# Optimization experiments

Hardware: AMD Instinct MI355X
Metric: run time of the kernel (lower is better)

## Reference

```python
import jax, jax.numpy as jnp
import numpy as np

B, S, D_MODEL, H = 2, 2048, 1024, 16
HD = D_MODEL // H  # 64
THETA = 10000.0


def setup_inputs() -> dict:
    key = jax.random.key(0)
    ks = jax.random.split(key, 5)
    std = (2.0 / (D_MODEL + D_MODEL)) ** 0.5
    x = jax.random.normal(ks[0], (B, S, D_MODEL), dtype=jnp.float32)
    Wq = jax.random.normal(ks[1], (D_MODEL, D_MODEL), dtype=jnp.float32) * std
    Wk = jax.random.normal(ks[2], (D_MODEL, D_MODEL), dtype=jnp.float32) * std
    Wv = jax.random.normal(ks[3], (D_MODEL, D_MODEL), dtype=jnp.float32) * std
    Wo = jax.random.normal(ks[4], (D_MODEL, D_MODEL), dtype=jnp.float32) * std
    # RoPE tables (buffers)
    pos = jnp.arange(S, dtype=jnp.float32)
    freq = THETA ** (-jnp.arange(0, HD, 2, dtype=jnp.float32) / HD)  # [HD/2]
    ang = jnp.outer(pos, freq)  # [S, HD/2]
    token_positions = jnp.arange(S, dtype=jnp.int32)
    return {
        "x": x,
        "token_positions": token_positions,
        "use_rope": 1,
        "Wq": Wq, "Wk": Wk, "Wv": Wv, "Wo": Wo,
        "cos": jnp.cos(ang), "sin": jnp.sin(ang),
    }


def _apply_rope(t, c, sn):
    # t: [b,h,s,d]; c,sn: [s,d/2] (broadcast over b,h)
    e = t[..., 0::2]
    o = t[..., 1::2]
    return jnp.stack([e * c - o * sn, o * c + e * sn], axis=-1).reshape(t.shape)


def reference(x, token_positions, use_rope, Wq, Wk, Wv, Wo, cos, sin):
    b, s, _ = x.shape

    def split_heads(t):  # [b,s,D] -> [b,h,s,hd]
        return t.reshape(b, s, H, HD).transpose(0, 2, 1, 3)

    q = split_heads(x @ Wq.T)
    k = split_heads(x @ Wk.T)
    v = split_heads(x @ Wv.T)

    if use_rope:
        c = cos[token_positions]   # [s, hd/2]
        sn = sin[token_positions]  # [s, hd/2]
        q = _apply_rope(q, c, sn)
        k = _apply_rope(k, c, sn)

    scale = 1.0 / jnp.sqrt(jnp.float32(HD))
    scores = jnp.einsum('bhqd,bhkd->bhqk', q, k) * scale  # [b,h,s,s]
    causal = jnp.tril(jnp.ones((s, s), dtype=bool))
    scores = jnp.where(causal, scores, -jnp.inf)
    attn = jax.nn.softmax(scores, axis=-1)
    y = jnp.einsum('bhqk,bhkd->bhqd', attn, v)
    y = y.transpose(0, 2, 1, 3).reshape(b, s, D_MODEL)
    return y @ Wo.T
```

## Files before the change

kernel.cpp:

```cpp
#include <hip/hip_runtime.h>
#include <math.h>

#define BB 2
#define SS 2048
#define DM 1024
#define NH 16
#define HD 64

typedef __attribute__((ext_vector_type(8))) __bf16 bf16x8;
typedef __attribute__((ext_vector_type(4))) __bf16 bf16x4;
typedef __attribute__((ext_vector_type(8))) unsigned short u16x8;
typedef __attribute__((ext_vector_type(4))) float f32x4;
typedef unsigned short u16;
typedef unsigned int u32;
typedef __attribute__((address_space(1))) unsigned int u32g;
typedef __attribute__((address_space(3))) unsigned int u32l;

#define CEXP 0.18033688011112042f

static __device__ __forceinline__ u16 f2bf(float f) {
    __bf16 h = (__bf16)f;
    return __builtin_bit_cast(unsigned short, h);
}

static __device__ __forceinline__ void gld16(const u16* g, u16* l) {
    __builtin_amdgcn_global_load_lds((const u32g*)g, (u32l*)l, 16, 0, 0);
}

__global__ __launch_bounds__(256)
void cast_all(const float* __restrict__ x,
              const float* __restrict__ wq, const float* __restrict__ wk,
              const float* __restrict__ wv, const float* __restrict__ wo,
              u16* __restrict__ xb, u16* __restrict__ wqb, u16* __restrict__ wkb,
              u16* __restrict__ wvb, u16* __restrict__ wob)
{
    const int N4X = (BB * SS * DM) / 4;
    const int N4W = (DM * DM) / 4;
    int i = blockIdx.x * 256 + threadIdx.x;
    const float* src; u16* dst; int off;
    if (i < N4X) { src = x; dst = xb; off = i; }
    else {
        int i2 = i - N4X;
        int w = i2 >> 18;
        off = i2 & (N4W - 1);
        switch (w) {
            case 0:  src = wq; dst = wqb; break;
            case 1:  src = wk; dst = wkb; break;
            case 2:  src = wv; dst = wvb; break;
            default: src = wo; dst = wob; break;
        }
    }
    float4 v = ((const float4*)src)[off];
    ushort4 o;
    o.x = f2bf(v.x); o.y = f2bf(v.y); o.z = f2bf(v.z); o.w = f2bf(v.w);
    ((ushort4*)dst)[off] = o;
}

__global__ __launch_bounds__(256, 3)
void qkv_gemm(const u16* __restrict__ X,
              const u16* __restrict__ Wq, const u16* __restrict__ Wk,
              const u16* __restrict__ Wv,
              const int* __restrict__ tp, const float* __restrict__ cosp,
              const float* __restrict__ sinp, const int* __restrict__ use_rope,
              u16* __restrict__ Q, u16* __restrict__ K, u16* __restrict__ V)
{
    const u16* W; u16* dst;
    if (blockIdx.z == 0)      { W = Wq; dst = Q; }
    else if (blockIdx.z == 1) { W = Wk; dst = K; }
    else                      { W = Wv; dst = V; }

    __shared__ u16 SH[4 * 64 * 68];
    u16* As = SH;
    u16* Bs = SH + 8192;
    const int t  = threadIdx.x;
    const int wv = t >> 6, L = t & 63, ln = L & 15, qd = L >> 4;
    const int i0 = blockIdx.y * 128, j0 = blockIdx.x * 128;
    const int wm = (wv >> 1) * 64, wn = (wv & 1) * 64;
    const int srow = L >> 3;
    const int scg  = ((L & 7) ^ (L >> 3)) * 8;

    f32x4 acc[4][4];
    #pragma unroll
    for (int a = 0; a < 4; ++a)
        #pragma unroll
        for (int b = 0; b < 4; ++b)
            #pragma unroll
            for (int e = 0; e < 4; ++e) acc[a][b][e] = 0.f;

    for (int k0 = 0; k0 < DM; k0 += 64) {
        __syncthreads();
        #pragma unroll
        for (int g = 0; g < 4; ++g) {
            int rb = wv * 32 + g * 8;
            gld16(X + (size_t)(i0 + rb + srow) * DM + k0 + scg, &As[rb * 64]);
            gld16(W + (size_t)(j0 + rb + srow) * DM + k0 + scg, &Bs[rb * 64]);
        }
        __syncthreads();
        bf16x8 a[4][2], b[4][2];
        #pragma unroll
        for (int mi = 0; mi < 4; ++mi)
            #pragma unroll
            for (int kd = 0; kd < 2; ++kd)
                a[mi][kd] = *(const bf16x8*)&As[(wm + mi * 16 + ln) * 64 + (((kd * 4 + qd) ^ (ln & 7)) * 8)];
        #pragma unroll
        for (int ni = 0; ni < 4; ++ni)
            #pragma unroll
            for (int kd = 0; kd < 2; ++kd)
                b[ni][kd] = *(const bf16x8*)&Bs[(wn + ni * 16 + ln) * 64 + (((kd * 4 + qd) ^ (ln & 7)) * 8)];
        #pragma unroll
        for (int kd = 0; kd < 2; ++kd)
            #pragma unroll
            for (int mi = 0; mi < 4; ++mi)
                #pragma unroll
                for (int ni = 0; ni < 4; ++ni)
                    acc[mi][ni] = __builtin_amdgcn_mfma_f32_16x16x32_bf16(a[mi][kd], b[ni][kd], acc[mi][ni], 0, 0, 0);
    }

    const int rope_on = (blockIdx.z < 2) ? use_rope[0] : 0;
    if (rope_on) {
        #pragma unroll
        for (int mi = 0; mi < 4; ++mi)
            #pragma unroll
            for (int r = 0; r < 4; ++r) {
                int gi = i0 + wm + mi * 16 + qd * 4 + r;
                int s = gi & 2047;
                int pos = tp[s];
                #pragma unroll
                for (int ni = 0; ni < 4; ++ni) {
                    int d = wn + ni * 16 + ln;
                    int dh = d & 63;
                    float c  = cosp[pos * 32 + (dh >> 1)];
                    float sn = sinp[pos * 32 + (dh >> 1)];
                    float v = acc[mi][ni][r];
                    float pv = __shfl_xor(v, 1);
                    acc[mi][ni][r] = (dh & 1) ? (v * c + pv * sn) : (v * c - pv * sn);
                }
            }
    }

    __syncthreads();
    u16* Ts = SH + wv * (64 * 68);
    #pragma unroll
    for (int mi = 0; mi < 4; ++mi)
        #pragma unroll
        for (int ni = 0; ni < 4; ++ni)
            #pragma unroll
            for (int r = 0; r < 4; ++r)
                Ts[(mi * 16 + qd * 4 + r) * 68 + ni * 16 + ln] = f2bf(acc[mi][ni][r]);

    const int h  = blockIdx.x * 2 + (wv & 1);
    const int sb = i0 + wm;
    const int b_ = sb >> 11, s0 = sb & 2047;
    if (blockIdx.z < 2) {
        const int lrow = L >> 3, lcol = (L & 7) * 8;
        #pragma unroll
        for (int r2 = 0; r2 < 8; ++r2) {
            int row = lrow + r2 * 8;
            u16x8 val = *(const u16x8*)&Ts[row * 68 + lcol];
            *(u16x8*)&dst[(((size_t)(b_ * NH + h)) * SS + s0 + row) * HD + lcol] = val;
        }
    } else {
        const int sch = (L & 7) * 8;
        const int dr0 = L >> 3;
        #pragma unroll
        for (int r2 = 0; r2 < 8; ++r2) {
            int d = dr0 + r2 * 8;
            u16x8 val;
            #pragma unroll
            for (int u = 0; u < 8; ++u) val[u] = Ts[(sch + u) * 68 + d];
            *(u16x8*)&dst[(((size_t)(b_ * NH + h)) * HD + d) * SS + s0 + sch] = val;
        }
    }
}

__global__ __launch_bounds__(512, 2)
void out_gemm(const u16* __restrict__ X, const u16* __restrict__ W,
              float* __restrict__ dst)
{
    __shared__ char SHB[73728];
    u16* As = (u16*)SHB;
    u16* Bs = (u16*)SHB + 8192;
    const int t  = threadIdx.x;
    const int wv = t >> 6, L = t & 63, ln = L & 15, qd = L >> 4;
    const int i0 = blockIdx.y * 128, j0 = blockIdx.x * 128;
    const int wm = (wv >> 2) * 64, wn = (wv & 3) * 32;
    const int srow = L >> 3;
    const int scg  = ((L & 7) ^ (L >> 3)) * 8;

    f32x4 acc[4][2];
    #pragma unroll
    for (int mi = 0; mi < 4; ++mi)
        #pragma unroll
        for (int ni = 0; ni < 2; ++ni)
            #pragma unroll
            for (int e = 0; e < 4; ++e) acc[mi][ni][e] = 0.f;

    for (int k0 = 0; k0 < DM; k0 += 64) {
        __syncthreads();
        #pragma unroll
        for (int g = 0; g < 2; ++g) {
            int rb = wv * 16 + g * 8;
            gld16(X + (size_t)(i0 + rb + srow) * DM + k0 + scg, &As[rb * 64]);
            gld16(W + (size_t)(j0 + rb + srow) * DM + k0 + scg, &Bs[rb * 64]);
        }
        __syncthreads();
        bf16x8 a[4][2], b[2][2];
        #pragma unroll
        for (int mi = 0; mi < 4; ++mi)
            #pragma unroll
            for (int kd = 0; kd < 2; ++kd)
                a[mi][kd] = *(const bf16x8*)&As[(wm + mi * 16 + ln) * 64 + (((kd * 4 + qd) ^ (ln & 7)) * 8)];
        #pragma unroll
        for (int ni = 0; ni < 2; ++ni)
            #pragma unroll
            for (int kd = 0; kd < 2; ++kd)
                b[ni][kd] = *(const bf16x8*)&Bs[(wn + ni * 16 + ln) * 64 + (((kd * 4 + qd) ^ (ln & 7)) * 8)];
        #pragma unroll
        for (int kd = 0; kd < 2; ++kd)
            #pragma unroll
            for (int mi = 0; mi < 4; ++mi)
                #pragma unroll
                for (int ni = 0; ni < 2; ++ni)
                    acc[mi][ni] = __builtin_amdgcn_mfma_f32_16x16x32_bf16(a[mi][kd], b[ni][kd], acc[mi][ni], 0, 0, 0);
    }

    __syncthreads();
    float* Ts = (float*)SHB + wv * (64 * 36);
    #pragma unroll
    for (int mi = 0; mi < 4; ++mi)
        #pragma unroll
        for (int ni = 0; ni < 2; ++ni)
            #pragma unroll
            for (int r = 0; r < 4; ++r)
                Ts[(mi * 16 + qd * 4 + r) * 36 + ni * 16 + ln] = acc[mi][ni][r];

    const int lrow = L >> 3, lch = L & 7;
    #pragma unroll
    for (int r2 = 0; r2 < 8; ++r2) {
        int row = lrow + r2 * 8;
        float4 v = *(const float4*)&Ts[row * 36 + lch * 4];
        *(float4*)&dst[(size_t)(i0 + wm + row) * DM + j0 + wn + lch * 4] = v;
    }
}

static __device__ __forceinline__ void group_step(
    const u16* KsB, const bf16x8 qf[2], u16* psw,
    bool diag, int rowg, int j0, int ln, int qd,
    float& m, float& l, bf16x8& pf0, bf16x8& pf1)
{
    const int pm = 2 * (ln & 7);
    f32x4 s[4];
    __builtin_amdgcn_s_setprio(1);
    #pragma unroll
    for (int mt = 0; mt < 4; ++mt) {
        bf16x8 a0 = *(const bf16x8*)&KsB[(mt * 16 + ln) * 64 + ((qd ^ (ln & 7)) * 8)];
        bf16x8 a1 = *(const bf16x8*)&KsB[(mt * 16 + ln) * 64 + (((4 + qd) ^ (ln & 7)) * 8)];
        #pragma unroll
        for (int e = 0; e < 4; ++e) s[mt][e] = 0.f;
        s[mt] = __builtin_amdgcn_mfma_f32_16x16x32_bf16(a0, qf[0], s[mt], 0, 0, 0);
        s[mt] = __builtin_amdgcn_mfma_f32_16x16x32_bf16(a1, qf[1], s[mt], 0, 0, 0);
    }
    __builtin_amdgcn_s_setprio(0);
    if (diag) {
        #pragma unroll
        for (int mt = 0; mt < 4; ++mt)
            #pragma unroll
            for (int r = 0; r < 4; ++r)
                if (j0 + mt * 16 + qd * 4 + r > rowg) s[mt][r] = -3.0e38f;
    }

    float p[16];
    float nmc = m * CEXP;
    #pragma unroll
    for (int mt = 0; mt < 4; ++mt)
        #pragma unroll
        for (int r = 0; r < 4; ++r)
            p[mt * 4 + r] = exp2f(fmaf(s[mt][r], CEXP, -nmc));

    float rm = s[0][0];
    #pragma unroll
    for (int mt = 0; mt < 4; ++mt)
        #pragma unroll
        for (int r = 0; r < 4; ++r) rm = fmaxf(rm, s[mt][r]);
    rm = fmaxf(rm, __shfl_xor(rm, 16));
    rm = fmaxf(rm, __shfl_xor(rm, 32));

    if (__any((rm - m) * CEXP > 8.0f)) {
        float nm = fmaxf(m, rm);
        float alpha = exp2f((m - nm) * CEXP);
        nmc = nm * CEXP;
        #pragma unroll
        for (int mt = 0; mt < 4; ++mt)
            #pragma unroll
            for (int r = 0; r < 4; ++r)
                p[mt * 4 + r] = exp2f(fmaf(s[mt][r], CEXP, -nmc));
        l *= alpha;
        m = nm;
    }

    float rs = 0.f;
    #pragma unroll
    for (int mt = 0; mt < 4; ++mt) {
        bf16x4 pk;
        #pragma unroll
        for (int r = 0; r < 4; ++r) {
            rs += p[mt * 4 + r];
            pk[r] = (__bf16)p[mt * 4 + r];
        }
        *(bf16x4*)(psw + ln * 64 + ((mt * 4 + qd) ^ pm) * 4) = pk;
    }
    rs += __shfl_xor(rs, 16);
    rs += __shfl_xor(rs, 32);
    l += rs;
    pf0 = *(const bf16x8*)(psw + ln * 64 + ((qd * 2) ^ pm) * 4);
    pf1 = *(const bf16x8*)(psw + ln * 64 + ((8 + qd * 2) ^ pm) * 4);
}

__global__ __launch_bounds__(512, 4)
void attn_kernel(const u16* __restrict__ Q, const u16* __restrict__ K,
                 const u16* __restrict__ V, u16* __restrict__ Y)
{
    __shared__ u16 Ks[2][64 * 64];
    __shared__ u16 Vt[2][64 * 64];
    __shared__ u16 Ps[8][16 * 64];

    const int t  = threadIdx.x;
    const int wv = t >> 6, L = t & 63, ln = L & 15, qd = L >> 4;
    const int wsub = wv & 3, grp = wv >> 2;
    const int bh = blockIdx.x;
    const int y = blockIdx.y;
    const int p = (y < 8) ? y : (23 - y);
    const int qb = (grp ? (31 - p) : p) * 64;
    const u16* Qp = Q + (size_t)bh * SS * HD;
    const u16* Kp = K + (size_t)bh * SS * HD;
    const u16* Vp = V + (size_t)bh * HD * SS;
    const int srow = L >> 3;
    const int scg  = ((L & 7) ^ (L >> 3)) * 8;

    const int ntile   = 32 - p;
    const int myTiles = grp ? ntile : (p + 1);

    bf16x8 qf[2];
    {
        const u16* rq = Qp + (size_t)(qb + wsub * 16 + ln) * HD;
        qf[0] = *(const bf16x8*)(rq + qd * 8);
        qf[1] = *(const bf16x8*)(rq + 32 + qd * 8);
    }

    f32x4 o[4];
    #pragma unroll
    for (int ni = 0; ni < 4; ++ni)
        #pragma unroll
        for (int e = 0; e < 4; ++e) o[ni][e] = 0.f;
    float m = -3.0e38f, l = 0.f;

    gld16(Kp + (size_t)(wv * 8 + srow) * HD + scg, &Ks[0][(wv * 8) * 64]);
    gld16(Vp + (size_t)(wv * 8 + srow) * SS + scg, &Vt[0][(wv * 8) * 64]);
    __syncthreads();

    for (int tix = 0; tix < ntile; ++tix) {
        const int j0 = tix * 64;
        const int buf = tix & 1;
        const bool more = (tix + 1 < ntile);

        if (more) {
            const int j1 = j0 + 64;
            gld16(Kp + (size_t)(j1 + wv * 8 + srow) * HD + scg, &Ks[buf ^ 1][(wv * 8) * 64]);
            gld16(Vp + (size_t)(wv * 8 + srow) * SS + j1 + scg, &Vt[buf ^ 1][(wv * 8) * 64]);
        }

        if (tix < myTiles) {
            bf16x8 vf[2][4];
            #pragma unroll
            for (int kc = 0; kc < 2; ++kc)
                #pragma unroll
                for (int ni = 0; ni < 4; ++ni)
                    vf[kc][ni] = *(const bf16x8*)&Vt[buf][(ni * 16 + ln) * 64 + (((kc * 4 + qd) ^ (ln & 7)) * 8)];

            float m_old = m;
            bf16x8 pf0, pf1;
            group_step(Ks[buf], qf, &Ps[wv][0], tix == myTiles - 1,
                       qb + wsub * 16 + ln, j0, ln, qd, m, l, pf0, pf1);
            if (m != m_old) {
                float alpha = exp2f((m_old - m) * CEXP);
                #pragma unroll
                for (int ni = 0; ni < 4; ++ni)
                    #pragma unroll
                    for (int r = 0; r < 4; ++r) o[ni][r] *= alpha;
            }
            __builtin_amdgcn_s_setprio(1);
            #pragma unroll
            for (int ni = 0; ni < 4; ++ni)
                o[ni] = __builtin_amdgcn_mfma_f32_16x16x32_bf16(vf[0][ni], pf0, o[ni], 0, 0, 0);
            #pragma unroll
            for (int ni = 0; ni < 4; ++ni)
                o[ni] = __builtin_amdgcn_mfma_f32_16x16x32_bf16(vf[1][ni], pf1, o[ni], 0, 0, 0);
            __builtin_amdgcn_s_setprio(0);
        }
        __syncthreads();
    }

    const int b = bh >> 4, h = bh & 15;
    const float inv = 1.f / l;
    const int sq = qb + wsub * 16 + ln;
    #pragma unroll
    for (int ni = 0; ni < 4; ++ni) {
        bf16x4 pk;
        #pragma unroll
        for (int r = 0; r < 4; ++r) pk[r] = (__bf16)(o[ni][r] * inv);
        *(bf16x4*)&Y[((size_t)(b * SS + sq)) * DM + h * HD + ni * 16 + qd * 4] = pk;
    }
}

extern "C" void kernel_launch(void* const* d_in, const int* in_sizes, int n_in,
                              void* d_out, int out_size, void* d_ws, size_t ws_size,
                              hipStream_t stream)
{
    const float* x        = (const float*)d_in[0];
    const int*   tp       = (const int*)d_in[1];
    const int*   use_rope = (const int*)d_in[2];
    const float* Wq       = (const float*)d_in[3];
    const float* Wk       = (const float*)d_in[4];
    const float* Wv       = (const float*)d_in[5];
    const float* Wo       = (const float*)d_in[6];
    const float* cosp     = (const float*)d_in[7];
    const float* sinp     = (const float*)d_in[8];
    float* out = (float*)d_out;

    char* ws = (char*)d_ws;
    const size_t MB = 1 << 20;
    u16* xb  = (u16*)(ws);
    u16* Wqb = (u16*)(ws + 8 * MB);
    u16* Wkb = (u16*)(ws + 10 * MB);
    u16* Wvb = (u16*)(ws + 12 * MB);
    u16* Wob = (u16*)(ws + 14 * MB);
    u16* Qb  = (u16*)(ws + 16 * MB);
    u16* Kb  = (u16*)(ws + 24 * MB);
    u16* Vb  = (u16*)(ws + 32 * MB);
    u16* Yb  = (u16*)(ws + 40 * MB);

    cast_all<<<8192, 256, 0, stream>>>(x, Wq, Wk, Wv, Wo, xb, Wqb, Wkb, Wvb, Wob);
    qkv_gemm<<<dim3(DM / 128, BB * SS / 128, 3), 256, 0, stream>>>(
        xb, Wqb, Wkb, Wvb, tp, cosp, sinp, use_rope, Qb, Kb, Vb);
    attn_kernel<<<dim3(BB * NH, 16), 512, 0, stream>>>(Qb, Kb, Vb, Yb);
    out_gemm<<<dim3(DM / 128, BB * SS / 128), 512, 0, stream>>>(Yb, Wob, out);
}
```

Baseline: 183.2 us.

## Split causal attention KV range across paired waves and read K/V directly

Each wave now owns a 16-row query strip. It processes the first half of the KV tiles for one strip and the second half for the mirrored strip. Partial softmax state (m, l, O) goes to shared memory and is merged with a partner wave, which balances causal work per wave. The double-buffered LDS staging of K and V tiles is removed in favour of direct global/L1 loads, and the grid becomes 32×32 blocks of 256 threads. This trades away the shared-memory reuse and prefetch overlap, exposing more global-load latency, in exchange for finer-grained, better-balanced work and lower LDS usage.

```diff
diff --git a/kernel.cpp b/kernel.cpp
--- a/kernel.cpp
+++ b/kernel.cpp
@@ -243,24 +243,23 @@
     }
 }
 
-static __device__ __forceinline__ void group_step(
-    const u16* KsB, const bf16x8 qf[2], u16* psw,
-    bool diag, int rowg, int j0, int ln, int qd,
-    float& m, float& l, bf16x8& pf0, bf16x8& pf1)
+static __device__ __forceinline__ void attn_tile(
+    const u16* __restrict__ Kp, const u16* __restrict__ Vp,
+    bf16x8 qf0, bf16x8 qf1, u16* psw,
+    int j0, bool diag, int rowg, int ln, int qd,
+    float& m, float& l, f32x4* o)
 {
     const int pm = 2 * (ln & 7);
     f32x4 s[4];
-    __builtin_amdgcn_s_setprio(1);
+    const u16* kb = Kp + (size_t)(j0 + ln) * HD + qd * 8;
     #pragma unroll
     for (int mt = 0; mt < 4; ++mt) {
-        bf16x8 a0 = *(const bf16x8*)&KsB[(mt * 16 + ln) * 64 + ((qd ^ (ln & 7)) * 8)];
-        bf16x8 a1 = *(const bf16x8*)&KsB[(mt * 16 + ln) * 64 + (((4 + qd) ^ (ln & 7)) * 8)];
-        #pragma unroll
-        for (int e = 0; e < 4; ++e) s[mt][e] = 0.f;
-        s[mt] = __builtin_amdgcn_mfma_f32_16x16x32_bf16(a0, qf[0], s[mt], 0, 0, 0);
-        s[mt] = __builtin_amdgcn_mfma_f32_16x16x32_bf16(a1, qf[1], s[mt], 0, 0, 0);
-    }
-    __builtin_amdgcn_s_setprio(0);
+        bf16x8 a0 = *(const bf16x8*)(kb + mt * 16 * HD);
+        bf16x8 a1 = *(const bf16x8*)(kb + mt * 16 * HD + 32);
+        s[mt][0] = s[mt][1] = s[mt][2] = s[mt][3] = 0.f;
+        s[mt] = __builtin_amdgcn_mfma_f32_16x16x32_bf16(a0, qf0, s[mt], 0, 0, 0);
+        s[mt] = __builtin_amdgcn_mfma_f32_16x16x32_bf16(a1, qf1, s[mt], 0, 0, 0);
+    }
     if (diag) {
         #pragma unroll
         for (int mt = 0; mt < 4; ++mt)
@@ -294,6 +293,10 @@
             #pragma unroll
             for (int r = 0; r < 4; ++r)
                 p[mt * 4 + r] = exp2f(fmaf(s[mt][r], CEXP, -nmc));
+        #pragma unroll
+        for (int ni = 0; ni < 4; ++ni)
+            #pragma unroll
+            for (int r = 0; r < 4; ++r) o[ni][r] *= alpha;
         l *= alpha;
         m = nm;
     }
@@ -312,103 +315,94 @@
     rs += __shfl_xor(rs, 16);
     rs += __shfl_xor(rs, 32);
     l += rs;
-    pf0 = *(const bf16x8*)(psw + ln * 64 + ((qd * 2) ^ pm) * 4);
-    pf1 = *(const bf16x8*)(psw + ln * 64 + ((8 + qd * 2) ^ pm) * 4);
-}
-
-__global__ __launch_bounds__(512, 4)
+    bf16x8 pf0 = *(const bf16x8*)(psw + ln * 64 + ((qd * 2) ^ pm) * 4);
+    bf16x8 pf1 = *(const bf16x8*)(psw + ln * 64 + ((8 + qd * 2) ^ pm) * 4);
+
+    const u16* vb = Vp + (size_t)ln * SS + j0 + qd * 8;
+    #pragma unroll
+    for (int ni = 0; ni < 4; ++ni) {
+        bf16x8 vf0 = *(const bf16x8*)(vb + (size_t)(ni * 16) * SS);
+        bf16x8 vf1 = *(const bf16x8*)(vb + (size_t)(ni * 16) * SS + 32);
+        o[ni] = __builtin_amdgcn_mfma_f32_16x16x32_bf16(vf0, pf0, o[ni], 0, 0, 0);
+        o[ni] = __builtin_amdgcn_mfma_f32_16x16x32_bf16(vf1, pf1, o[ni], 0, 0, 0);
+    }
+}
+
+__global__ __launch_bounds__(256, 4)
 void attn_kernel(const u16* __restrict__ Q, const u16* __restrict__ K,
                  const u16* __restrict__ V, u16* __restrict__ Y)
 {
-    __shared__ u16 Ks[2][64 * 64];
-    __shared__ u16 Vt[2][64 * 64];
-    __shared__ u16 Ps[8][16 * 64];
+    __shared__ u16  Ps[4][16 * 64];
+    __shared__ float MO[4][16 * 64];
+    __shared__ float ML[4][32];
 
     const int t  = threadIdx.x;
     const int wv = t >> 6, L = t & 63, ln = L & 15, qd = L >> 4;
-    const int wsub = wv & 3, grp = wv >> 2;
-    const int bh = blockIdx.x;
-    const int y = blockIdx.y;
-    const int p = (y < 8) ? y : (23 - y);
-    const int qb = (grp ? (31 - p) : p) * 64;
+    const int bh = blockIdx.x, b2 = blockIdx.y;
+    const int b  = bh >> 4, h = bh & 15;
     const u16* Qp = Q + (size_t)bh * SS * HD;
     const u16* Kp = K + (size_t)bh * SS * HD;
     const u16* Vp = V + (size_t)bh * HD * SS;
-    const int srow = L >> 3;
-    const int scg  = ((L & 7) ^ (L >> 3)) * 8;
-
-    const int ntile   = 32 - p;
-    const int myTiles = grp ? ntile : (p + 1);
-
-    bf16x8 qf[2];
+
+    const int s1 = (wv == 0) ? 2 * b2 : (wv == 1) ? 2 * b2 + 1
+                 : (wv == 2) ? 126 - 2 * b2 : 127 - 2 * b2;
+    const int s2 = 127 - s1;
+    const int T1 = (s1 >> 2) + 1, T2 = (s2 >> 2) + 1;
+
+    u16* psw = &Ps[wv][0];
+    float m, l;
+    f32x4 o[4];
+
     {
-        const u16* rq = Qp + (size_t)(qb + wsub * 16 + ln) * HD;
-        qf[0] = *(const bf16x8*)(rq + qd * 8);
-        qf[1] = *(const bf16x8*)(rq + 32 + qd * 8);
-    }
-
-    f32x4 o[4];
-    #pragma unroll
-    for (int ni = 0; ni < 4; ++ni)
-        #pragma unroll
-        for (int e = 0; e < 4; ++e) o[ni][e] = 0.f;
-    float m = -3.0e38f, l = 0.f;
-
-    gld16(Kp + (size_t)(wv * 8 + srow) * HD + scg, &Ks[0][(wv * 8) * 64]);
-    gld16(Vp + (size_t)(wv * 8 + srow) * SS + scg, &Vt[0][(wv * 8) * 64]);
+        const int qb = s1 * 16;
+        const u16* rq = Qp + (size_t)(qb + ln) * HD;
+        bf16x8 qf0 = *(const bf16x8*)(rq + qd * 8);
+        bf16x8 qf1 = *(const bf16x8*)(rq + 32 + qd * 8);
+        m = -3.0e38f; l = 0.f;
+        #pragma unroll
+        for (int ni = 0; ni < 4; ++ni)
+            o[ni][0] = o[ni][1] = o[ni][2] = o[ni][3] = 0.f;
+        const int e1 = T1 >> 1;
+        #pragma unroll 1
+        for (int tix = 0; tix < e1; ++tix)
+            attn_tile(Kp, Vp, qf0, qf1, psw, tix * 64, false, qb + ln, ln, qd, m, l, o);
+        if (qd == 0) { ML[wv][ln] = m; ML[wv][16 + ln] = l; }
+        #pragma unroll
+        for (int ni = 0; ni < 4; ++ni)
+            *(f32x4*)&MO[wv][ln * 64 + (((ni * 4 + qd) ^ ln) * 4)] = o[ni];
+    }
+
+    {
+        const int qb = s2 * 16;
+        const u16* rq = Qp + (size_t)(qb + ln) * HD;
+        bf16x8 qf0 = *(const bf16x8*)(rq + qd * 8);
+        bf16x8 qf1 = *(const bf16x8*)(rq + 32 + qd * 8);
+        m = -3.0e38f; l = 0.f;
+        #pragma unroll 1
+        for (int tix = T2 >> 1; tix < T2; ++tix)
+            attn_tile(Kp, Vp, qf0, qf1, psw, tix * 64, tix == T2 - 1, qb + ln, ln, qd, m, l, o);
+    }
+
     __syncthreads();
 
-    for (int tix = 0; tix < ntile; ++tix) {
-        const int j0 = tix * 64;
-        const int buf = tix & 1;
-        const bool more = (tix + 1 < ntile);
-
-        if (more) {
-            const int j1 = j0 + 64;
-            gld16(Kp + (size_t)(j1 + wv * 8 + srow) * HD + scg, &Ks[buf ^ 1][(wv * 8) * 64]);
-            gld16(Vp + (size_t)(wv * 8 + srow) * SS + j1 + scg, &Vt[buf ^ 1][(wv * 8) * 64]);
-        }
-
-        if (tix < myTiles) {
-            bf16x8 vf[2][4];
-            #pragma unroll
-            for (int kc = 0; kc < 2; ++kc)
-                #pragma unroll
-                for (int ni = 0; ni < 4; ++ni)
-                    vf[kc][ni] = *(const bf16x8*)&Vt[buf][(ni * 16 + ln) * 64 + (((kc * 4 + qd) ^ (ln & 7)) * 8)];
-
-            float m_old = m;
-            bf16x8 pf0, pf1;
-            group_step(Ks[buf], qf, &Ps[wv][0], tix == myTiles - 1,
-                       qb + wsub * 16 + ln, j0, ln, qd, m, l, pf0, pf1);
-            if (m != m_old) {
-                float alpha = exp2f((m_old - m) * CEXP);
-                #pragma unroll
-                for (int ni = 0; ni < 4; ++ni)
-                    #pragma unroll
-                    for (int r = 0; r < 4; ++r) o[ni][r] *= alpha;
-            }
-            __builtin_amdgcn_s_setprio(1);
-            #pragma unroll
-            for (int ni = 0; ni < 4; ++ni)
-                o[ni] = __builtin_amdgcn_mfma_f32_16x16x32_bf16(vf[0][ni], pf0, o[ni], 0, 0, 0);
-            #pragma unroll
-            for (int ni = 0; ni < 4; ++ni)
-                o[ni] = __builtin_amdgcn_mfma_f32_16x16x32_bf16(vf[1][ni], pf1, o[ni], 0, 0, 0);
-            __builtin_amdgcn_s_setprio(0);
-        }
-        __syncthreads();
-    }
-
-    const int b = bh >> 4, h = bh & 15;
-    const float inv = 1.f / l;
-    const int sq = qb + wsub * 16 + ln;
-    #pragma unroll
-    for (int ni = 0; ni < 4; ++ni) {
-        bf16x4 pk;
-        #pragma unroll
-        for (int r = 0; r < 4; ++r) pk[r] = (__bf16)(o[ni][r] * inv);
-        *(bf16x4*)&Y[((size_t)(b * SS + sq)) * DM + h * HD + ni * 16 + qd * 4] = pk;
+    {
+        const int pw = 3 - wv;
+        float mp = ML[pw][ln], lp = ML[pw][16 + ln];
+        float mf = fmaxf(m, mp);
+        float as = exp2f((m - mf) * CEXP);
+        float ap = exp2f((mp - mf) * CEXP);
+        float lf = as * l + ap * lp;
+        float inv = 1.f / lf;
+        const int sq = s2 * 16 + ln;
+        #pragma unroll
+        for (int ni = 0; ni < 4; ++ni) {
+            f32x4 op = *(const f32x4*)&MO[pw][ln * 64 + (((ni * 4 + qd) ^ ln) * 4)];
+            bf16x4 pk;
+            #pragma unroll
+            for (int r = 0; r < 4; ++r)
+                pk[r] = (__bf16)((as * o[ni][r] + ap * op[r]) * inv);
+            *(bf16x4*)&Y[((size_t)(b * SS + sq)) * DM + h * HD + ni * 16 + qd * 4] = pk;
+        }
     }
 }
 
@@ -442,6 +436,6 @@
     cast_all<<<8192, 256, 0, stream>>>(x, Wq, Wk, Wv, Wo, xb, Wqb, Wkb, Wvb, Wob);
     qkv_gemm<<<dim3(DM / 128, BB * SS / 128, 3), 256, 0, stream>>>(
         xb, Wqb, Wkb, Wvb, tp, cosp, sinp, use_rope, Qb, Kb, Vb);
-    attn_kernel<<<dim3(BB * NH, 16), 512, 0, stream>>>(Qb, Kb, Vb, Yb);
+    attn_kernel<<<dim3(BB * NH, 32), 256, 0, stream>>>(Qb, Kb, Vb, Yb);
     out_gemm<<<dim3(DM / 128, BB * SS / 128), 512, 0, stream>>>(Yb, Wob, out);
 }
```

New measurement: 262.5 us. 43.3% more time.

## Exchange P fragments via cross-lane shuffles and write V transpose directly

Applied to the files above, without the earlier changes.

In the attention kernel, the softmax probabilities are packed into bf16 pairs and redistributed into the MFMA B-operand layout with lane shuffles, replacing the per-wave LDS staging buffer. This removes the LDS write/read round trip and frees shared memory, at the cost of 16 shuffle instructions and extra selects per tile. Separately, the QKV projection kernel now writes the transposed V output straight from accumulator registers as 4-element bf16 stores. That skips the LDS transpose and its barrier, but makes the global stores narrower and more scattered.

```diff
diff --git a/kernel.cpp b/kernel.cpp
--- a/kernel.cpp
+++ b/kernel.cpp
@@ -11,6 +11,7 @@
 typedef __attribute__((ext_vector_type(4))) __bf16 bf16x4;
 typedef __attribute__((ext_vector_type(8))) unsigned short u16x8;
 typedef __attribute__((ext_vector_type(4))) float f32x4;
+typedef __attribute__((ext_vector_type(4))) unsigned int u32x4;
 typedef unsigned short u16;
 typedef unsigned int u32;
 typedef __attribute__((address_space(1))) unsigned int u32g;
@@ -21,6 +22,11 @@
 static __device__ __forceinline__ u16 f2bf(float f) {
     __bf16 h = (__bf16)f;
     return __builtin_bit_cast(unsigned short, h);
+}
+
+static __device__ __forceinline__ u32 pk2(float a, float b) {
+    u32 lo = (u32)f2bf(a), hi = (u32)f2bf(b);
+    return lo | (hi << 16);
 }
 
 static __device__ __forceinline__ void gld16(const u16* g, u16* l) {
@@ -138,20 +144,20 @@
             }
     }
 
-    __syncthreads();
-    u16* Ts = SH + wv * (64 * 68);
-    #pragma unroll
-    for (int mi = 0; mi < 4; ++mi)
-        #pragma unroll
-        for (int ni = 0; ni < 4; ++ni)
-            #pragma unroll
-            for (int r = 0; r < 4; ++r)
-                Ts[(mi * 16 + qd * 4 + r) * 68 + ni * 16 + ln] = f2bf(acc[mi][ni][r]);
-
     const int h  = blockIdx.x * 2 + (wv & 1);
     const int sb = i0 + wm;
     const int b_ = sb >> 11, s0 = sb & 2047;
     if (blockIdx.z < 2) {
+        __syncthreads();
+        u16* Ts = SH + wv * (64 * 68);
+        #pragma unroll
+        for (int mi = 0; mi < 4; ++mi)
+            #pragma unroll
+            for (int ni = 0; ni < 4; ++ni)
+                #pragma unroll
+                for (int r = 0; r < 4; ++r)
+                    Ts[(mi * 16 + qd * 4 + r) * 68 + ni * 16 + ln] = f2bf(acc[mi][ni][r]);
+
         const int lrow = L >> 3, lcol = (L & 7) * 8;
         #pragma unroll
         for (int r2 = 0; r2 < 8; ++r2) {
@@ -160,16 +166,16 @@
             *(u16x8*)&dst[(((size_t)(b_ * NH + h)) * SS + s0 + row) * HD + lcol] = val;
         }
     } else {
-        const int sch = (L & 7) * 8;
-        const int dr0 = L >> 3;
-        #pragma unroll
-        for (int r2 = 0; r2 < 8; ++r2) {
-            int d = dr0 + r2 * 8;
-            u16x8 val;
-            #pragma unroll
-            for (int u = 0; u < 8; ++u) val[u] = Ts[(sch + u) * 68 + d];
-            *(u16x8*)&dst[(((size_t)(b_ * NH + h)) * HD + d) * SS + s0 + sch] = val;
-        }
+        #pragma unroll
+        for (int mi = 0; mi < 4; ++mi)
+            #pragma unroll
+            for (int ni = 0; ni < 4; ++ni) {
+                bf16x4 pk;
+                #pragma unroll
+                for (int r = 0; r < 4; ++r) pk[r] = (__bf16)acc[mi][ni][r];
+                *(bf16x4*)&dst[(((size_t)(b_ * NH + h)) * HD + ni * 16 + ln) * SS
+                               + s0 + mi * 16 + qd * 4] = pk;
+            }
     }
 }
 
@@ -244,11 +250,10 @@
 }
 
 static __device__ __forceinline__ void group_step(
-    const u16* KsB, const bf16x8 qf[2], u16* psw,
-    bool diag, int rowg, int j0, int ln, int qd,
+    const u16* KsB, const bf16x8 qf[2],
+    bool diag, int rowg, int j0, int ln, int qd, int srcA,
     float& m, float& l, bf16x8& pf0, bf16x8& pf1)
 {
-    const int pm = 2 * (ln & 7);
     f32x4 s[4];
     __builtin_amdgcn_s_setprio(1);
     #pragma unroll
@@ -298,22 +303,35 @@
         m = nm;
     }
 
+    u32 P00 = pk2(p[0],  p[1]),  P01 = pk2(p[2],  p[3]);
+    u32 P10 = pk2(p[4],  p[5]),  P11 = pk2(p[6],  p[7]);
+    u32 P20 = pk2(p[8],  p[9]),  P21 = pk2(p[10], p[11]);
+    u32 P30 = pk2(p[12], p[13]), P31 = pk2(p[14], p[15]);
+    const int srcB = srcA + 16;
+    int a00 = __shfl((int)P00, srcA), a10 = __shfl((int)P10, srcA);
+    int a01 = __shfl((int)P01, srcA), a11 = __shfl((int)P11, srcA);
+    int b00 = __shfl((int)P00, srcB), b10 = __shfl((int)P10, srcB);
+    int b01 = __shfl((int)P01, srcB), b11 = __shfl((int)P11, srcB);
+    int a20 = __shfl((int)P20, srcA), a30 = __shfl((int)P30, srcA);
+    int a21 = __shfl((int)P21, srcA), a31 = __shfl((int)P31, srcA);
+    int b20 = __shfl((int)P20, srcB), b30 = __shfl((int)P30, srcB);
+    int b21 = __shfl((int)P21, srcB), b31 = __shfl((int)P31, srcB);
+
     float rs = 0.f;
     #pragma unroll
-    for (int mt = 0; mt < 4; ++mt) {
-        bf16x4 pk;
-        #pragma unroll
-        for (int r = 0; r < 4; ++r) {
-            rs += p[mt * 4 + r];
-            pk[r] = (__bf16)p[mt * 4 + r];
-        }
-        *(bf16x4*)(psw + ln * 64 + ((mt * 4 + qd) ^ pm) * 4) = pk;
-    }
+    for (int i = 0; i < 16; ++i) rs += p[i];
     rs += __shfl_xor(rs, 16);
     rs += __shfl_xor(rs, 32);
     l += rs;
-    pf0 = *(const bf16x8*)(psw + ln * 64 + ((qd * 2) ^ pm) * 4);
-    pf1 = *(const bf16x8*)(psw + ln * 64 + ((8 + qd * 2) ^ pm) * 4);
+
+    const bool hi2 = (qd >> 1) != 0;
+    u32x4 f0, f1;
+    f0[0] = (u32)(hi2 ? a10 : a00); f0[1] = (u32)(hi2 ? a11 : a01);
+    f0[2] = (u32)(hi2 ? b10 : b00); f0[3] = (u32)(hi2 ? b11 : b01);
+    f1[0] = (u32)(hi2 ? a30 : a20); f1[1] = (u32)(hi2 ? a31 : a21);
+    f1[2] = (u32)(hi2 ? b30 : b20); f1[3] = (u32)(hi2 ? b31 : b21);
+    pf0 = __builtin_bit_cast(bf16x8, f0);
+    pf1 = __builtin_bit_cast(bf16x8, f1);
 }
 
 __global__ __launch_bounds__(512, 4)
@@ -322,7 +340,6 @@
 {
     __shared__ u16 Ks[2][64 * 64];
     __shared__ u16 Vt[2][64 * 64];
-    __shared__ u16 Ps[8][16 * 64];
 
     const int t  = threadIdx.x;
     const int wv = t >> 6, L = t & 63, ln = L & 15, qd = L >> 4;
@@ -336,6 +353,7 @@
     const u16* Vp = V + (size_t)bh * HD * SS;
     const int srow = L >> 3;
     const int scg  = ((L & 7) ^ (L >> 3)) * 8;
+    const int srcA = ln + 32 * (qd & 1);
 
     const int ntile   = 32 - p;
     const int myTiles = grp ? ntile : (p + 1);
@@ -379,8 +397,8 @@
 
             float m_old = m;
             bf16x8 pf0, pf1;
-            group_step(Ks[buf], qf, &Ps[wv][0], tix == myTiles - 1,
-                       qb + wsub * 16 + ln, j0, ln, qd, m, l, pf0, pf1);
+            group_step(Ks[buf], qf, tix == myTiles - 1,
+                       qb + wsub * 16 + ln, j0, ln, qd, srcA, m, l, pf0, pf1);
             if (m != m_old) {
                 float alpha = exp2f((m_old - m) * CEXP);
                 #pragma unroll
```

After: 189.0 us. +3.1%, slower.
